# Optimization experiments

Measured on AMD Instinct MI355X. Metric: run time of the kernel, lower is better.

Reference implementation:

```python
import jax, jax.numpy as jnp
import numpy as np

SIGMA = 10.0   # collision energy scale (init sigma)
LCOL = 0.5     # collision length scale (init lcol)


def setup_inputs() -> dict:
    key = jax.random.key(0)
    B, D = 64, 2050  # 64 chains, N = 1 + (D-4)/2 = 1024 beads each
    # values must be in [-0.5, 0.5]: r2 = conf + 0.5 feeds arccos(1 - 2*r2)
    confdata = jax.random.uniform(key, (B, D), dtype=jnp.float32, minval=-0.5, maxval=0.5)
    return {"confdata": confdata}


def _energy(confdata):
    # --- get_poly, batched over all chains ---
    init_pos = confdata[:, 1:4]                      # [B, 3]
    c = confdata[:, 4:] + 0.5                        # [B, 2*(N-1)] in [0, 1]
    r1, r2 = c[:, ::2], c[:, 1::2]                   # [B, N-1]
    ph = r1 * (2.0 * jnp.pi)
    th = jnp.arccos(1.0 - 2.0 * r2)
    st = jnp.sin(th)
    steps = jnp.stack([st * jnp.cos(ph), st * jnp.sin(ph), jnp.cos(th)], axis=-1)  # [B, N-1, 3]
    pos = jnp.cumsum(jnp.concatenate([init_pos[:, None, :], steps], axis=1), axis=1)  # [B, N, 3]

    # --- collisions: sum over pairs with d > 0 of exp(-(d/lcol)^2) ---
    diff = pos[:, :, None, :] - pos[:, None, :, :]   # [B, N, N, 3]; exact zeros on diagonal
    d2 = jnp.sum(diff * diff, axis=-1)               # [B, N, N]
    e = jnp.where(d2 > 0, jnp.exp(-d2 / (LCOL * LCOL)), 0.0)
    return SIGMA * jnp.sum(e)


def reference(confdata):
    return _energy(confdata)
```

## Files before the change

### kernel.cpp

```cpp
#include <hip/hip_runtime.h>

#define NPOS 1024
#define NBATCH 64
#define DROW 2050
#define T 8
#define TS 128
#define NPG 18
#define NBLK (NBATCH * NPG)

__global__ __launch_bounds__(256) void fused_kernel(const float* __restrict__ conf,
                                                    float* __restrict__ part) {
  __shared__ float4 P[NPOS];
  __shared__ float wx[4], wy[4], wz[4];
  __shared__ float red[4];

  const int g = blockIdx.x % NPG;
  const int b = blockIdx.x / NPG;
  const int tid = threadIdx.x;
  const int lane = tid & 63, w = tid >> 6;
  const float* __restrict__ row = conf + b * DROW;
  const float ALPHA = 2.40224481f;

  float lx[4], ly[4], lz[4];
  float rx = 0.f, ry = 0.f, rz = 0.f;
#pragma unroll
  for (int k = 0; k < 4; ++k) {
    const int n = 4 * tid + k;
    if (n > 0) {
      const float2 rr = *reinterpret_cast<const float2*>(row + 2 + 2 * n);
      const float r1 = rr.x + 0.5f;
      const float r2 = rr.y + 0.5f;
      const float ct = 1.f - 2.f * r2;
      const float st = sqrtf(fmaxf(0.f, 1.f - ct * ct));
      const float sp = __builtin_amdgcn_sinf(r1);
      const float cp = __builtin_amdgcn_cosf(r1);
      rx += st * cp; ry += st * sp; rz += ct;
    }
    lx[k] = rx; ly[k] = ry; lz[k] = rz;
  }
  const float tx = rx, ty = ry, tz = rz;
  float sx = rx, sy = ry, sz = rz;
#pragma unroll
  for (int off = 1; off < 64; off <<= 1) {
    const float ax = __shfl_up(sx, off, 64);
    const float ay = __shfl_up(sy, off, 64);
    const float az = __shfl_up(sz, off, 64);
    if (lane >= off) { sx += ax; sy += ay; sz += az; }
  }
  if (lane == 63) { wx[w] = sx; wy[w] = sy; wz[w] = sz; }
  __syncthreads();
  float cx = 0.f, cy = 0.f, cz = 0.f;
#pragma unroll
  for (int ww = 0; ww < 3; ++ww)
    if (ww < w) { cx += wx[ww]; cy += wy[ww]; cz += wz[ww]; }

  const float ox = row[1] + cx + (sx - tx);
  const float oy = row[2] + cy + (sy - ty);
  const float oz = row[3] + cz + (sz - tz);
#pragma unroll
  for (int k = 0; k < 4; ++k) {
    P[4 * tid + k] = make_float4(ALPHA * (ox + lx[k]), ALPHA * (oy + ly[k]),
                                 ALPHA * (oz + lz[k]), 0.f);
  }
  __syncthreads();

  const int sub = tid >> 7;
  const int t2 = tid & 127;

  float a0 = 0.f, a1 = 0.f, a2 = 0.f, a3 = 0.f;

  if (g < 4) {
    const int ti = 2 * g + sub;
    const float4* __restrict__ PT = &P[ti * TS];
    const float4 pi = PT[t2];
#pragma unroll 4
    for (int jj = 1; jj <= 60; jj += 4) {
      const float4 q0 = PT[(t2 + jj + 0) & 127];
      const float4 q1 = PT[(t2 + jj + 1) & 127];
      const float4 q2 = PT[(t2 + jj + 2) & 127];
      const float4 q3 = PT[(t2 + jj + 3) & 127];
      float dx, dy, dz, d2;
      dx = pi.x - q0.x; dy = pi.y - q0.y; dz = pi.z - q0.z;
      d2 = dx * dx + dy * dy + dz * dz; a0 += __builtin_amdgcn_exp2f(-d2);
      dx = pi.x - q1.x; dy = pi.y - q1.y; dz = pi.z - q1.z;
      d2 = dx * dx + dy * dy + dz * dz; a1 += __builtin_amdgcn_exp2f(-d2);
      dx = pi.x - q2.x; dy = pi.y - q2.y; dz = pi.z - q2.z;
      d2 = dx * dx + dy * dy + dz * dz; a2 += __builtin_amdgcn_exp2f(-d2);
      dx = pi.x - q3.x; dy = pi.y - q3.y; dz = pi.z - q3.z;
      d2 = dx * dx + dy * dy + dz * dz; a3 += __builtin_amdgcn_exp2f(-d2);
    }
#pragma unroll
    for (int jj = 61; jj <= 63; ++jj) {
      const float4 q = PT[(t2 + jj) & 127];
      const float dx = pi.x - q.x, dy = pi.y - q.y, dz = pi.z - q.z;
      const float d2 = dx * dx + dy * dy + dz * dz;
      a0 += __builtin_amdgcn_exp2f(-d2);
    }
    {
      const float4 q = PT[(t2 + 64) & 127];
      const float dx = pi.x - q.x, dy = pi.y - q.y, dz = pi.z - q.z;
      const float d2 = dx * dx + dy * dy + dz * dz;
      a1 += (t2 < 64) ? __builtin_amdgcn_exp2f(-d2) : 0.f;
    }
  } else {
    int rem = 2 * (g - 4) + sub;
    int ti = 0;
    while (rem >= T - 1 - ti) { rem -= T - 1 - ti; ++ti; }
    const int tj = ti + 1 + rem;
    const float4 pi = P[ti * TS + t2];
    const float4* __restrict__ PJ = &P[tj * TS];
#pragma unroll 4
    for (int jj = 0; jj < TS; jj += 4) {
      const float4 q0 = PJ[jj + 0];
      const float4 q1 = PJ[jj + 1];
      const float4 q2 = PJ[jj + 2];
      const float4 q3 = PJ[jj + 3];
      float dx, dy, dz, d2;
      dx = pi.x - q0.x; dy = pi.y - q0.y; dz = pi.z - q0.z;
      d2 = dx * dx + dy * dy + dz * dz; a0 += __builtin_amdgcn_exp2f(-d2);
      dx = pi.x - q1.x; dy = pi.y - q1.y; dz = pi.z - q1.z;
      d2 = dx * dx + dy * dy + dz * dz; a1 += __builtin_amdgcn_exp2f(-d2);
      dx = pi.x - q2.x; dy = pi.y - q2.y; dz = pi.z - q2.z;
      d2 = dx * dx + dy * dy + dz * dz; a2 += __builtin_amdgcn_exp2f(-d2);
      dx = pi.x - q3.x; dy = pi.y - q3.y; dz = pi.z - q3.z;
      d2 = dx * dx + dy * dy + dz * dz; a3 += __builtin_amdgcn_exp2f(-d2);
    }
  }

  float acc = (a0 + a1) + (a2 + a3);
#pragma unroll
  for (int off = 32; off; off >>= 1) acc += __shfl_down(acc, off, 64);
  if (lane == 0) red[w] = acc;
  __syncthreads();
  if (tid == 0) part[blockIdx.x] = (red[0] + red[1]) + (red[2] + red[3]);
}

__global__ __launch_bounds__(256) void reduce_kernel(const float* __restrict__ part,
                                                     float* __restrict__ out) {
  float s = 0.f;
  for (int i = threadIdx.x; i < NBLK; i += 256) s += part[i];
#pragma unroll
  for (int off = 32; off; off >>= 1) s += __shfl_down(s, off, 64);
  __shared__ float red[4];
  const int lane = threadIdx.x & 63, w = threadIdx.x >> 6;
  if (lane == 0) red[w] = s;
  __syncthreads();
  if (threadIdx.x == 0)
    out[0] = 20.0f * ((red[0] + red[1]) + (red[2] + red[3]));
}

extern "C" void kernel_launch(void* const* d_in, const int* in_sizes, int n_in,
                              void* d_out, int out_size, void* d_ws, size_t ws_size,
                              hipStream_t stream) {
  const float* conf = (const float*)d_in[0];
  float* out = (float*)d_out;
  float* part = (float*)d_ws;
  hipLaunchKernelGGL(fused_kernel, dim3(NBLK), dim3(256), 0, stream, conf, part);
  hipLaunchKernelGGL(reduce_kernel, dim3(1), dim3(256), 0, stream, part, out);
}
```

Baseline: 22.59 us.

## Compute full pair matrix via expanded-norm dot products with 4-row register blocking

Drops the upper-triangle tiling and computes the full N×N pair sum. Each block takes a half of the i rows and a chunk of the j columns, and each thread holds four i positions in registers. Squared distances come from precomputed negative norms plus a doubled dot product, so each pair costs a few FMAs before the exp. The diagonal is removed by subtracting a fixed constant in the final reduction instead of masking it. In exchange the kernel evaluates roughly twice as many exponentials, the expanded form adds cancellation error, and the constant assumes every diagonal term is exactly one.

```diff
diff --git a/kernel.cpp b/kernel.cpp
--- a/kernel.cpp
+++ b/kernel.cpp
@@ -3,10 +3,8 @@
 #define NPOS 1024
 #define NBATCH 64
 #define DROW 2050
-#define T 8
-#define TS 128
-#define NPG 18
-#define NBLK (NBATCH * NPG)
+#define JCH 8
+#define NBLK (NBATCH * 2 * JCH)
 
 __global__ __launch_bounds__(256) void fused_kernel(const float* __restrict__ conf,
                                                     float* __restrict__ part) {
@@ -14,8 +12,10 @@
   __shared__ float wx[4], wy[4], wz[4];
   __shared__ float red[4];
 
-  const int g = blockIdx.x % NPG;
-  const int b = blockIdx.x / NPG;
+  const int g = blockIdx.x % (2 * JCH);
+  const int b = blockIdx.x / (2 * JCH);
+  const int ih = g >> 3;
+  const int jc = g & 7;
   const int tid = threadIdx.x;
   const int lane = tid & 63, w = tid >> 6;
   const float* __restrict__ row = conf + b * DROW;
@@ -59,72 +59,34 @@
   const float oz = row[3] + cz + (sz - tz);
 #pragma unroll
   for (int k = 0; k < 4; ++k) {
-    P[4 * tid + k] = make_float4(ALPHA * (ox + lx[k]), ALPHA * (oy + ly[k]),
-                                 ALPHA * (oz + lz[k]), 0.f);
+    const float X = ALPHA * (ox + lx[k]);
+    const float Y = ALPHA * (oy + ly[k]);
+    const float Z = ALPHA * (oz + lz[k]);
+    float n2 = X * X; n2 = fmaf(Y, Y, n2); n2 = fmaf(Z, Z, n2);
+    P[4 * tid + k] = make_float4(X, Y, Z, -n2);
   }
   __syncthreads();
 
-  const int sub = tid >> 7;
-  const int t2 = tid & 127;
+  const int tl = tid & 127;
+  const int half = tid >> 7;
+  const float4 pi0 = P[ih * 512 + tl];
+  const float4 pi1 = P[ih * 512 + tl + 128];
+  const float4 pi2 = P[ih * 512 + tl + 256];
+  const float4 pi3 = P[ih * 512 + tl + 384];
+  const float4* __restrict__ PJ = &P[jc * 128 + half * 64];
 
   float a0 = 0.f, a1 = 0.f, a2 = 0.f, a3 = 0.f;
-
-  if (g < 4) {
-    const int ti = 2 * g + sub;
-    const float4* __restrict__ PT = &P[ti * TS];
-    const float4 pi = PT[t2];
 #pragma unroll 4
-    for (int jj = 1; jj <= 60; jj += 4) {
-      const float4 q0 = PT[(t2 + jj + 0) & 127];
-      const float4 q1 = PT[(t2 + jj + 1) & 127];
-      const float4 q2 = PT[(t2 + jj + 2) & 127];
-      const float4 q3 = PT[(t2 + jj + 3) & 127];
-      float dx, dy, dz, d2;
-      dx = pi.x - q0.x; dy = pi.y - q0.y; dz = pi.z - q0.z;
-      d2 = dx * dx + dy * dy + dz * dz; a0 += __builtin_amdgcn_exp2f(-d2);
-      dx = pi.x - q1.x; dy = pi.y - q1.y; dz = pi.z - q1.z;
-      d2 = dx * dx + dy * dy + dz * dz; a1 += __builtin_amdgcn_exp2f(-d2);
-      dx = pi.x - q2.x; dy = pi.y - q2.y; dz = pi.z - q2.z;
-      d2 = dx * dx + dy * dy + dz * dz; a2 += __builtin_amdgcn_exp2f(-d2);
-      dx = pi.x - q3.x; dy = pi.y - q3.y; dz = pi.z - q3.z;
-      d2 = dx * dx + dy * dy + dz * dz; a3 += __builtin_amdgcn_exp2f(-d2);
-    }
-#pragma unroll
-    for (int jj = 61; jj <= 63; ++jj) {
-      const float4 q = PT[(t2 + jj) & 127];
-      const float dx = pi.x - q.x, dy = pi.y - q.y, dz = pi.z - q.z;
-      const float d2 = dx * dx + dy * dy + dz * dz;
-      a0 += __builtin_amdgcn_exp2f(-d2);
-    }
-    {
-      const float4 q = PT[(t2 + 64) & 127];
-      const float dx = pi.x - q.x, dy = pi.y - q.y, dz = pi.z - q.z;
-      const float d2 = dx * dx + dy * dy + dz * dz;
-      a1 += (t2 < 64) ? __builtin_amdgcn_exp2f(-d2) : 0.f;
-    }
-  } else {
-    int rem = 2 * (g - 4) + sub;
-    int ti = 0;
-    while (rem >= T - 1 - ti) { rem -= T - 1 - ti; ++ti; }
-    const int tj = ti + 1 + rem;
-    const float4 pi = P[ti * TS + t2];
-    const float4* __restrict__ PJ = &P[tj * TS];
-#pragma unroll 4
-    for (int jj = 0; jj < TS; jj += 4) {
-      const float4 q0 = PJ[jj + 0];
-      const float4 q1 = PJ[jj + 1];
-      const float4 q2 = PJ[jj + 2];
-      const float4 q3 = PJ[jj + 3];
-      float dx, dy, dz, d2;
-      dx = pi.x - q0.x; dy = pi.y - q0.y; dz = pi.z - q0.z;
-      d2 = dx * dx + dy * dy + dz * dz; a0 += __builtin_amdgcn_exp2f(-d2);
-      dx = pi.x - q1.x; dy = pi.y - q1.y; dz = pi.z - q1.z;
-      d2 = dx * dx + dy * dy + dz * dz; a1 += __builtin_amdgcn_exp2f(-d2);
-      dx = pi.x - q2.x; dy = pi.y - q2.y; dz = pi.z - q2.z;
-      d2 = dx * dx + dy * dy + dz * dz; a2 += __builtin_amdgcn_exp2f(-d2);
-      dx = pi.x - q3.x; dy = pi.y - q3.y; dz = pi.z - q3.z;
-      d2 = dx * dx + dy * dy + dz * dz; a3 += __builtin_amdgcn_exp2f(-d2);
-    }
+  for (int jj = 0; jj < 64; ++jj) {
+    const float4 q = PJ[jj];
+    float t0 = pi0.x * q.x; t0 = fmaf(pi0.y, q.y, t0); t0 = fmaf(pi0.z, q.z, t0);
+    float t1 = pi1.x * q.x; t1 = fmaf(pi1.y, q.y, t1); t1 = fmaf(pi1.z, q.z, t1);
+    float t2 = pi2.x * q.x; t2 = fmaf(pi2.y, q.y, t2); t2 = fmaf(pi2.z, q.z, t2);
+    float t3 = pi3.x * q.x; t3 = fmaf(pi3.y, q.y, t3); t3 = fmaf(pi3.z, q.z, t3);
+    a0 += __builtin_amdgcn_exp2f(fmaf(2.f, t0, pi0.w + q.w));
+    a1 += __builtin_amdgcn_exp2f(fmaf(2.f, t1, pi1.w + q.w));
+    a2 += __builtin_amdgcn_exp2f(fmaf(2.f, t2, pi2.w + q.w));
+    a3 += __builtin_amdgcn_exp2f(fmaf(2.f, t3, pi3.w + q.w));
   }
 
   float acc = (a0 + a1) + (a2 + a3);
@@ -145,8 +107,9 @@
   const int lane = threadIdx.x & 63, w = threadIdx.x >> 6;
   if (lane == 0) red[w] = s;
   __syncthreads();
-  if (threadIdx.x == 0)
-    out[0] = 20.0f * ((red[0] + red[1]) + (red[2] + red[3]));
+  if (threadIdx.x == 0) {
+    out[0] = 10.0f * ((red[0] + red[1]) + (red[2] + red[3])) - 655360.0f;
+  }
 }
 
 extern "C" void kernel_launch(void* const* d_in, const int* in_sizes, int n_in,
```

Result: slower. 23.54 us (+4.2%).
